# Kernel optimization log

Measured on AMD Instinct MI355X. Metric: run time of the kernel, lower is better.

Reference implementation:

```python
import jax, jax.numpy as jnp
import numpy as np

B, S, UNITS = 32, 2048, 512

def setup_inputs() -> dict:
    key = jax.random.key(0)
    ks = jax.random.split(key, 8)
    sc = 1.0 / np.sqrt(UNITS)
    return {
        "s_prev": jax.random.normal(ks[0], (B, UNITS), jnp.float32),
        "hidden_states": jax.random.normal(ks[1], (B, S, UNITS), jnp.float32),
        "W_kernel": jax.random.normal(ks[2], (UNITS, UNITS), jnp.float32) * sc,
        "W_bias": jnp.zeros((UNITS,), jnp.float32),
        "U_kernel": jax.random.normal(ks[3], (UNITS, UNITS), jnp.float32) * sc,
        "U_bias": jnp.zeros((UNITS,), jnp.float32),
        "V_kernel": jax.random.normal(ks[4], (UNITS, 1), jnp.float32) * sc,
        "V_bias": jnp.zeros((1,), jnp.float32),
    }

def reference(s_prev, hidden_states, W_kernel, W_bias, U_kernel, U_bias, V_kernel, V_bias):
    # NOTE: faithful to the source code: U is applied to s_prev, W to hidden_states,
    # and the context is computed as softmax-weights * s_prev (as written, a quirk
    # of the original module), summed over the sequence axis.
    first = s_prev @ U_kernel + U_bias                      # (B, units)
    second = hidden_states @ W_kernel + W_bias              # (B, S, units)
    score = jnp.tanh(first[:, None, :] + second) @ V_kernel + V_bias  # (B, S, 1)
    weights = jax.nn.softmax(score, axis=1)                 # (B, S, 1)
    context = jnp.sum(weights * s_prev[:, None, :], axis=1) # (B, units)
    return context, weights
```

## Files before the change

kernel.cpp:

```cpp
#include <hip/hip_runtime.h>

#define NBATCH 32
#define SEQ    2048
#define NU     512
#define ASTR   36

typedef __attribute__((ext_vector_type(8)))  short bf16x8;
typedef __attribute__((ext_vector_type(16))) float f32x16;

__device__ __forceinline__ short bf16_of(float f) {
  union { float f; unsigned u; } v; v.f = f;
  unsigned r = v.u + 0x7fffu + ((v.u >> 16) & 1u);
  return (short)(r >> 16);
}

__device__ __forceinline__ float fast_tanh(float x) {
  float ax = __builtin_fabsf(x);
  float t  = __expf(-2.0f * ax);
  float r  = (1.0f - t) / (1.0f + t);
  return x < 0.0f ? -r : r;
}

__global__ __launch_bounds__(256) void prep_w(const float* __restrict__ W,
                                              short* __restrict__ Wt) {
  int idx = blockIdx.x * 256 + threadIdx.x;
  int u = idx >> 9, k = idx & 511;
  Wt[(size_t)u * NU + k] = bf16_of(W[(size_t)k * NU + u]);
}

__global__ __launch_bounds__(256) void prep_first(const float* __restrict__ sp,
                                                  const float* __restrict__ U,
                                                  const float* __restrict__ Ub,
                                                  const float* __restrict__ Wb,
                                                  float* __restrict__ first) {
  __shared__ float srow[NU];
  int b = blockIdx.x >> 1;
  int half = blockIdx.x & 1;
  int t = threadIdx.x;
  srow[t]       = sp[b * NU + t];
  srow[t + 256] = sp[b * NU + t + 256];
  __syncthreads();
  int col = half * 256 + t;
  float acc = Ub[col] + Wb[col];
  #pragma unroll 8
  for (int k = 0; k < NU; ++k) acc += srow[k] * U[(size_t)k * NU + col];
  first[b * NU + col] = acc;
}

__global__ __launch_bounds__(256, 3) void attn_main(
    const float* __restrict__ h,
    const short* __restrict__ Wt,
    const float* __restrict__ first,
    const float* __restrict__ V,
    float* __restrict__ s0)
{
  __shared__ short Alds[2][128 * ASTR];
  __shared__ short Blds[2][128 * ASTR];
  __shared__ float scores_lds[128];

  const int tid  = threadIdx.x;
  const int lane = tid & 63;
  const int w    = tid >> 6;
  const int wr   = w >> 1, wc = w & 1;
  const int l31  = lane & 31, hi = lane >> 5;

  const int bid = blockIdx.x;
  const int lb  = (bid & 7) * 256 + (bid >> 3);
  const int panel = lb >> 2, q = lb & 3;
  const int rowbase = panel * 128;
  const int b = panel >> 4;

  const int arow  = tid >> 1;
  const int ahalf = tid & 1;
  const float* hA = h + (size_t)(rowbase + arow) * NU + ahalf * 16;
  const int awr   = arow * ASTR + ahalf * 16;
  const short* bsrc = Wt + (size_t)(q * 128 + arow) * NU + ahalf * 16;
  const int bwr   = awr;

  const int rA0 = (wr * 64 +  0 + l31) * ASTR + hi * 8;
  const int rA1 = (wr * 64 + 32 + l31) * ASTR + hi * 8;
  const int rB0 = (wc * 64 +  0 + l31) * ASTR + hi * 8;
  const int rB1 = (wc * 64 + 32 + l31) * ASTR + hi * 8;

  f32x16 acc[2][2];
  #pragma unroll
  for (int rt = 0; rt < 2; ++rt)
    #pragma unroll
    for (int ct = 0; ct < 2; ++ct)
      #pragma unroll
      for (int r = 0; r < 16; ++r) acc[rt][ct][r] = 0.f;

  float4 r0, r1, r2, r3;
  int4 q0, q1;

  r0 = *reinterpret_cast<const float4*>(hA + 0);
  r1 = *reinterpret_cast<const float4*>(hA + 4);
  r2 = *reinterpret_cast<const float4*>(hA + 8);
  r3 = *reinterpret_cast<const float4*>(hA + 12);
  q0 = *reinterpret_cast<const int4*>(bsrc + 0);
  q1 = *reinterpret_cast<const int4*>(bsrc + 8);
  {
    bf16x8 v0, v1;
    v0[0]=bf16_of(r0.x); v0[1]=bf16_of(r0.y); v0[2]=bf16_of(r0.z); v0[3]=bf16_of(r0.w);
    v0[4]=bf16_of(r1.x); v0[5]=bf16_of(r1.y); v0[6]=bf16_of(r1.z); v0[7]=bf16_of(r1.w);
    v1[0]=bf16_of(r2.x); v1[1]=bf16_of(r2.y); v1[2]=bf16_of(r2.z); v1[3]=bf16_of(r2.w);
    v1[4]=bf16_of(r3.x); v1[5]=bf16_of(r3.y); v1[6]=bf16_of(r3.z); v1[7]=bf16_of(r3.w);
    *reinterpret_cast<bf16x8*>(&Alds[0][awr])     = v0;
    *reinterpret_cast<bf16x8*>(&Alds[0][awr + 8]) = v1;
    *reinterpret_cast<int4*>(&Blds[0][bwr])       = q0;
    *reinterpret_cast<int4*>(&Blds[0][bwr + 8])   = q1;
  }
  __syncthreads();

  for (int kt = 0; kt < 16; ++kt) {
    const int cur = kt & 1;
    if (kt < 15) {
      const float* hk = hA + (kt + 1) * 32;
      r0 = *reinterpret_cast<const float4*>(hk + 0);
      r1 = *reinterpret_cast<const float4*>(hk + 4);
      r2 = *reinterpret_cast<const float4*>(hk + 8);
      r3 = *reinterpret_cast<const float4*>(hk + 12);
      const short* bk = bsrc + (kt + 1) * 32;
      q0 = *reinterpret_cast<const int4*>(bk + 0);
      q1 = *reinterpret_cast<const int4*>(bk + 8);
    }

    #pragma unroll
    for (int ks = 0; ks < 2; ++ks) {
      bf16x8 af[2], bf[2];
      af[0] = *reinterpret_cast<const bf16x8*>(&Alds[cur][rA0 + ks * 16]);
      af[1] = *reinterpret_cast<const bf16x8*>(&Alds[cur][rA1 + ks * 16]);
      bf[0] = *reinterpret_cast<const bf16x8*>(&Blds[cur][rB0 + ks * 16]);
      bf[1] = *reinterpret_cast<const bf16x8*>(&Blds[cur][rB1 + ks * 16]);
      #pragma unroll
      for (int rt = 0; rt < 2; ++rt)
        #pragma unroll
        for (int ct = 0; ct < 2; ++ct)
          acc[rt][ct] = __builtin_amdgcn_mfma_f32_32x32x16_bf16(af[rt], bf[ct], acc[rt][ct], 0, 0, 0);
    }

    if (kt < 15) {
      bf16x8 v0, v1;
      v0[0]=bf16_of(r0.x); v0[1]=bf16_of(r0.y); v0[2]=bf16_of(r0.z); v0[3]=bf16_of(r0.w);
      v0[4]=bf16_of(r1.x); v0[5]=bf16_of(r1.y); v0[6]=bf16_of(r1.z); v0[7]=bf16_of(r1.w);
      v1[0]=bf16_of(r2.x); v1[1]=bf16_of(r2.y); v1[2]=bf16_of(r2.z); v1[3]=bf16_of(r2.w);
      v1[4]=bf16_of(r3.x); v1[5]=bf16_of(r3.y); v1[6]=bf16_of(r3.z); v1[7]=bf16_of(r3.w);
      const int nxt = cur ^ 1;
      *reinterpret_cast<bf16x8*>(&Alds[nxt][awr])     = v0;
      *reinterpret_cast<bf16x8*>(&Alds[nxt][awr + 8]) = v1;
      *reinterpret_cast<int4*>(&Blds[nxt][bwr])       = q0;
      *reinterpret_cast<int4*>(&Blds[nxt][bwr + 8])   = q1;
    }
    __syncthreads();
  }

  float fv[2], vv[2];
  #pragma unroll
  for (int ct = 0; ct < 2; ++ct) {
    int col = q * 128 + wc * 64 + ct * 32 + l31;
    fv[ct] = first[b * NU + col];
    vv[ct] = V[col];
  }
  float part[2][16];
  #pragma unroll
  for (int rt = 0; rt < 2; ++rt) {
    #pragma unroll
    for (int r = 0; r < 16; ++r) {
      float p = 0.f;
      #pragma unroll
      for (int ct = 0; ct < 2; ++ct)
        p += vv[ct] * fast_tanh(fv[ct] + acc[rt][ct][r]);
      #pragma unroll
      for (int m = 1; m < 32; m <<= 1) p += __shfl_xor(p, m, 64);
      part[rt][r] = p;
    }
  }
  __syncthreads();
  if (wc == 0 && l31 == 0) {
    #pragma unroll
    for (int rt = 0; rt < 2; ++rt)
      #pragma unroll
      for (int r = 0; r < 16; ++r)
        scores_lds[wr * 64 + rt * 32 + (r & 3) + 8 * (r >> 2) + 4 * hi] = part[rt][r];
  }
  __syncthreads();
  if (wc == 1 && l31 == 0) {
    #pragma unroll
    for (int rt = 0; rt < 2; ++rt)
      #pragma unroll
      for (int r = 0; r < 16; ++r)
        scores_lds[wr * 64 + rt * 32 + (r & 3) + 8 * (r >> 2) + 4 * hi] += part[rt][r];
  }
  __syncthreads();
  if (tid < 128) atomicAdd(&s0[rowbase + tid], scores_lds[tid]);
}

__global__ __launch_bounds__(256) void softmax_ctx(const float* __restrict__ sp,
                                                   float* __restrict__ out) {
  const int b = blockIdx.x;
  const int t = threadIdx.x;
  float* wgt = out + NBATCH * NU + (size_t)b * SEQ;
  __shared__ float red[4];

  float v[8];
  float mx = -1e30f;
  #pragma unroll
  for (int i = 0; i < 8; ++i) { v[i] = wgt[t + i * 256]; mx = fmaxf(mx, v[i]); }
  #pragma unroll
  for (int m = 1; m < 64; m <<= 1) mx = fmaxf(mx, __shfl_xor(mx, m, 64));
  if ((t & 63) == 0) red[t >> 6] = mx;
  __syncthreads();
  mx = fmaxf(fmaxf(red[0], red[1]), fmaxf(red[2], red[3]));
  __syncthreads();

  float se = 0.f;
  #pragma unroll
  for (int i = 0; i < 8; ++i) { v[i] = __expf(v[i] - mx); se += v[i]; }
  #pragma unroll
  for (int m = 1; m < 64; m <<= 1) se += __shfl_xor(se, m, 64);
  if ((t & 63) == 0) red[t >> 6] = se;
  __syncthreads();
  se = red[0] + red[1] + red[2] + red[3];
  __syncthreads();

  const float inv = 1.0f / se;
  float sw = 0.f;
  #pragma unroll
  for (int i = 0; i < 8; ++i) { float wi = v[i] * inv; wgt[t + i * 256] = wi; sw += wi; }
  #pragma unroll
  for (int m = 1; m < 64; m <<= 1) sw += __shfl_xor(sw, m, 64);
  if ((t & 63) == 0) red[t >> 6] = sw;
  __syncthreads();
  sw = red[0] + red[1] + red[2] + red[3];

  out[b * NU + t]       = sp[b * NU + t] * sw;
  out[b * NU + t + 256] = sp[b * NU + t + 256] * sw;
}

extern "C" void kernel_launch(void* const* d_in, const int* in_sizes, int n_in,
                              void* d_out, int out_size, void* d_ws, size_t ws_size,
                              hipStream_t stream) {
  (void)in_sizes; (void)n_in; (void)out_size; (void)ws_size;
  const float* s_prev = (const float*)d_in[0];
  const float* h      = (const float*)d_in[1];
  const float* Wk     = (const float*)d_in[2];
  const float* Wb     = (const float*)d_in[3];
  const float* Uk     = (const float*)d_in[4];
  const float* Ub     = (const float*)d_in[5];
  const float* Vk     = (const float*)d_in[6];

  float* out   = (float*)d_out;
  float* first = (float*)d_ws;
  short* Wt    = (short*)((char*)d_ws + 65536);
  float* s0    = out + NBATCH * NU;

  hipMemsetAsync(s0, 0, (size_t)NBATCH * SEQ * sizeof(float), stream);
  prep_w     <<<1024, 256, 0, stream>>>(Wk, Wt);
  prep_first <<<  64, 256, 0, stream>>>(s_prev, Uk, Ub, Wb, first);
  attn_main  <<<2048, 256, 0, stream>>>(h, Wt, first, Vk, s0);
  softmax_ctx<<<  32, 256, 0, stream>>>(s_prev, out);
}
```

Measured before the change: 120.5 us.

## Prefetch h two tiles ahead, truncate bf16 via perm, merge prep kernels

The main GEMM loop now keeps two register sets of hidden-state data in flight, loading the tile two K-steps ahead with a manually unrolled ping-pong loop, so global-load latency is better hidden behind MFMA work. The float-to-bf16 conversion for the activations changes from round-to-nearest-even bit arithmetic to a single byte-permute truncation per pair, which cuts VALU work but lowers accuracy slightly. The two prep kernels are merged into one launch to save launch overhead. The extra prefetch registers may raise register pressure under the 3-blocks-per-CU launch bound.

```diff
diff --git a/kernel.cpp b/kernel.cpp
--- a/kernel.cpp
+++ b/kernel.cpp
@@ -8,10 +8,14 @@
 typedef __attribute__((ext_vector_type(8)))  short bf16x8;
 typedef __attribute__((ext_vector_type(16))) float f32x16;
 
-__device__ __forceinline__ short bf16_of(float f) {
+__device__ __forceinline__ short bf16_rne(float f) {
   union { float f; unsigned u; } v; v.f = f;
   unsigned r = v.u + 0x7fffu + ((v.u >> 16) & 1u);
   return (short)(r >> 16);
+}
+
+__device__ __forceinline__ unsigned pk2(float lo, float hi) {
+  return __builtin_amdgcn_perm(__float_as_uint(hi), __float_as_uint(lo), 0x07060302u);
 }
 
 __device__ __forceinline__ float fast_tanh(float x) {
@@ -21,30 +25,30 @@
   return x < 0.0f ? -r : r;
 }
 
-__global__ __launch_bounds__(256) void prep_w(const float* __restrict__ W,
-                                              short* __restrict__ Wt) {
-  int idx = blockIdx.x * 256 + threadIdx.x;
-  int u = idx >> 9, k = idx & 511;
-  Wt[(size_t)u * NU + k] = bf16_of(W[(size_t)k * NU + u]);
-}
-
-__global__ __launch_bounds__(256) void prep_first(const float* __restrict__ sp,
-                                                  const float* __restrict__ U,
-                                                  const float* __restrict__ Ub,
-                                                  const float* __restrict__ Wb,
-                                                  float* __restrict__ first) {
+__global__ __launch_bounds__(256) void prep_all(const float* __restrict__ W,
+                                                const float* __restrict__ sp,
+                                                const float* __restrict__ U,
+                                                const float* __restrict__ Ub,
+                                                const float* __restrict__ Wb,
+                                                short* __restrict__ Wt,
+                                                float* __restrict__ first) {
   __shared__ float srow[NU];
-  int b = blockIdx.x >> 1;
-  int half = blockIdx.x & 1;
-  int t = threadIdx.x;
-  srow[t]       = sp[b * NU + t];
-  srow[t + 256] = sp[b * NU + t + 256];
-  __syncthreads();
-  int col = half * 256 + t;
-  float acc = Ub[col] + Wb[col];
-  #pragma unroll 8
-  for (int k = 0; k < NU; ++k) acc += srow[k] * U[(size_t)k * NU + col];
-  first[b * NU + col] = acc;
+  if (blockIdx.x < 1024) {
+    int idx = blockIdx.x * 256 + threadIdx.x;
+    int u = idx >> 9, k = idx & 511;
+    Wt[(size_t)u * NU + k] = bf16_rne(W[(size_t)k * NU + u]);
+  } else {
+    int blk = blockIdx.x - 1024;
+    int b = blk >> 1, half = blk & 1, t = threadIdx.x;
+    srow[t]       = sp[b * NU + t];
+    srow[t + 256] = sp[b * NU + t + 256];
+    __syncthreads();
+    int col = half * 256 + t;
+    float acc = Ub[col] + Wb[col];
+    #pragma unroll 8
+    for (int k = 0; k < NU; ++k) acc += srow[k] * U[(size_t)k * NU + col];
+    first[b * NU + col] = acc;
+  }
 }
 
 __global__ __launch_bounds__(256, 3) void attn_main(
@@ -75,7 +79,6 @@
   const float* hA = h + (size_t)(rowbase + arow) * NU + ahalf * 16;
   const int awr   = arow * ASTR + ahalf * 16;
   const short* bsrc = Wt + (size_t)(q * 128 + arow) * NU + ahalf * 16;
-  const int bwr   = awr;
 
   const int rA0 = (wr * 64 +  0 + l31) * ASTR + hi * 8;
   const int rA1 = (wr * 64 + 32 + l31) * ASTR + hi * 8;
@@ -90,69 +93,89 @@
       #pragma unroll
       for (int r = 0; r < 16; ++r) acc[rt][ct][r] = 0.f;
 
-  float4 r0, r1, r2, r3;
-  int4 q0, q1;
-
-  r0 = *reinterpret_cast<const float4*>(hA + 0);
-  r1 = *reinterpret_cast<const float4*>(hA + 4);
-  r2 = *reinterpret_cast<const float4*>(hA + 8);
-  r3 = *reinterpret_cast<const float4*>(hA + 12);
-  q0 = *reinterpret_cast<const int4*>(bsrc + 0);
-  q1 = *reinterpret_cast<const int4*>(bsrc + 8);
-  {
-    bf16x8 v0, v1;
-    v0[0]=bf16_of(r0.x); v0[1]=bf16_of(r0.y); v0[2]=bf16_of(r0.z); v0[3]=bf16_of(r0.w);
-    v0[4]=bf16_of(r1.x); v0[5]=bf16_of(r1.y); v0[6]=bf16_of(r1.z); v0[7]=bf16_of(r1.w);
-    v1[0]=bf16_of(r2.x); v1[1]=bf16_of(r2.y); v1[2]=bf16_of(r2.z); v1[3]=bf16_of(r2.w);
-    v1[4]=bf16_of(r3.x); v1[5]=bf16_of(r3.y); v1[6]=bf16_of(r3.z); v1[7]=bf16_of(r3.w);
-    *reinterpret_cast<bf16x8*>(&Alds[0][awr])     = v0;
-    *reinterpret_cast<bf16x8*>(&Alds[0][awr + 8]) = v1;
-    *reinterpret_cast<int4*>(&Blds[0][bwr])       = q0;
-    *reinterpret_cast<int4*>(&Blds[0][bwr + 8])   = q1;
-  }
-  __syncthreads();
-
-  for (int kt = 0; kt < 16; ++kt) {
-    const int cur = kt & 1;
-    if (kt < 15) {
-      const float* hk = hA + (kt + 1) * 32;
-      r0 = *reinterpret_cast<const float4*>(hk + 0);
-      r1 = *reinterpret_cast<const float4*>(hk + 4);
-      r2 = *reinterpret_cast<const float4*>(hk + 8);
-      r3 = *reinterpret_cast<const float4*>(hk + 12);
-      const short* bk = bsrc + (kt + 1) * 32;
-      q0 = *reinterpret_cast<const int4*>(bk + 0);
-      q1 = *reinterpret_cast<const int4*>(bk + 8);
-    }
-
-    #pragma unroll
-    for (int ks = 0; ks < 2; ++ks) {
-      bf16x8 af[2], bf[2];
-      af[0] = *reinterpret_cast<const bf16x8*>(&Alds[cur][rA0 + ks * 16]);
-      af[1] = *reinterpret_cast<const bf16x8*>(&Alds[cur][rA1 + ks * 16]);
-      bf[0] = *reinterpret_cast<const bf16x8*>(&Blds[cur][rB0 + ks * 16]);
-      bf[1] = *reinterpret_cast<const bf16x8*>(&Blds[cur][rB1 + ks * 16]);
-      #pragma unroll
-      for (int rt = 0; rt < 2; ++rt)
-        #pragma unroll
-        for (int ct = 0; ct < 2; ++ct)
-          acc[rt][ct] = __builtin_amdgcn_mfma_f32_32x32x16_bf16(af[rt], bf[ct], acc[rt][ct], 0, 0, 0);
-    }
-
-    if (kt < 15) {
-      bf16x8 v0, v1;
-      v0[0]=bf16_of(r0.x); v0[1]=bf16_of(r0.y); v0[2]=bf16_of(r0.z); v0[3]=bf16_of(r0.w);
-      v0[4]=bf16_of(r1.x); v0[5]=bf16_of(r1.y); v0[6]=bf16_of(r1.z); v0[7]=bf16_of(r1.w);
-      v1[0]=bf16_of(r2.x); v1[1]=bf16_of(r2.y); v1[2]=bf16_of(r2.z); v1[3]=bf16_of(r2.w);
-      v1[4]=bf16_of(r3.x); v1[5]=bf16_of(r3.y); v1[6]=bf16_of(r3.z); v1[7]=bf16_of(r3.w);
-      const int nxt = cur ^ 1;
-      *reinterpret_cast<bf16x8*>(&Alds[nxt][awr])     = v0;
-      *reinterpret_cast<bf16x8*>(&Alds[nxt][awr + 8]) = v1;
-      *reinterpret_cast<int4*>(&Blds[nxt][bwr])       = q0;
-      *reinterpret_cast<int4*>(&Blds[nxt][bwr + 8])   = q1;
-    }
+  float4 ha0, ha1, ha2, ha3;
+  float4 hb0, hb1, hb2, hb3;
+  int4   bq0, bq1;
+
+  #define CVT_WRITE(dst, H0, H1, H2, H3)                                   \
+    {                                                                      \
+      uint4 u0, u1;                                                        \
+      u0.x = pk2(H0.x, H0.y); u0.y = pk2(H0.z, H0.w);                      \
+      u0.z = pk2(H1.x, H1.y); u0.w = pk2(H1.z, H1.w);                      \
+      u1.x = pk2(H2.x, H2.y); u1.y = pk2(H2.z, H2.w);                      \
+      u1.z = pk2(H3.x, H3.y); u1.w = pk2(H3.z, H3.w);                      \
+      *reinterpret_cast<uint4*>(&Alds[dst][awr])     = u0;                 \
+      *reinterpret_cast<uint4*>(&Alds[dst][awr + 8]) = u1;                 \
+      *reinterpret_cast<int4*>(&Blds[dst][awr])      = bq0;                \
+      *reinterpret_cast<int4*>(&Blds[dst][awr + 8])  = bq1;                \
+    }
+
+  #define COMPUTE(cur)                                                     \
+    _Pragma("unroll")                                                      \
+    for (int ks = 0; ks < 2; ++ks) {                                       \
+      bf16x8 af0, af1, bf0, bf1;                                           \
+      af0 = *reinterpret_cast<const bf16x8*>(&Alds[cur][rA0 + ks * 16]);   \
+      af1 = *reinterpret_cast<const bf16x8*>(&Alds[cur][rA1 + ks * 16]);   \
+      bf0 = *reinterpret_cast<const bf16x8*>(&Blds[cur][rB0 + ks * 16]);   \
+      bf1 = *reinterpret_cast<const bf16x8*>(&Blds[cur][rB1 + ks * 16]);   \
+      acc[0][0] = __builtin_amdgcn_mfma_f32_32x32x16_bf16(af0, bf0, acc[0][0], 0, 0, 0); \
+      acc[0][1] = __builtin_amdgcn_mfma_f32_32x32x16_bf16(af0, bf1, acc[0][1], 0, 0, 0); \
+      acc[1][0] = __builtin_amdgcn_mfma_f32_32x32x16_bf16(af1, bf0, acc[1][0], 0, 0, 0); \
+      acc[1][1] = __builtin_amdgcn_mfma_f32_32x32x16_bf16(af1, bf1, acc[1][1], 0, 0, 0); \
+    }
+
+  bq0 = *reinterpret_cast<const int4*>(bsrc);
+  bq1 = *reinterpret_cast<const int4*>(bsrc + 8);
+  ha0 = *reinterpret_cast<const float4*>(hA + 0);
+  ha1 = *reinterpret_cast<const float4*>(hA + 4);
+  ha2 = *reinterpret_cast<const float4*>(hA + 8);
+  ha3 = *reinterpret_cast<const float4*>(hA + 12);
+  CVT_WRITE(0, ha0, ha1, ha2, ha3);
+  hb0 = *reinterpret_cast<const float4*>(hA + 32);
+  hb1 = *reinterpret_cast<const float4*>(hA + 36);
+  hb2 = *reinterpret_cast<const float4*>(hA + 40);
+  hb3 = *reinterpret_cast<const float4*>(hA + 44);
+  __syncthreads();
+
+  for (int kt2 = 0; kt2 < 7; ++kt2) {
+    const int kt = kt2 * 2;
+    bq0 = *reinterpret_cast<const int4*>(bsrc + (kt + 1) * 32);
+    bq1 = *reinterpret_cast<const int4*>(bsrc + (kt + 1) * 32 + 8);
+    {
+      const float* p = hA + (kt + 2) * 32;
+      ha0 = *reinterpret_cast<const float4*>(p + 0);
+      ha1 = *reinterpret_cast<const float4*>(p + 4);
+      ha2 = *reinterpret_cast<const float4*>(p + 8);
+      ha3 = *reinterpret_cast<const float4*>(p + 12);
+    }
+    COMPUTE(0);
+    CVT_WRITE(1, hb0, hb1, hb2, hb3);
     __syncthreads();
-  }
+
+    bq0 = *reinterpret_cast<const int4*>(bsrc + (kt + 2) * 32);
+    bq1 = *reinterpret_cast<const int4*>(bsrc + (kt + 2) * 32 + 8);
+    {
+      const float* p = hA + (kt + 3) * 32;
+      hb0 = *reinterpret_cast<const float4*>(p + 0);
+      hb1 = *reinterpret_cast<const float4*>(p + 4);
+      hb2 = *reinterpret_cast<const float4*>(p + 8);
+      hb3 = *reinterpret_cast<const float4*>(p + 12);
+    }
+    COMPUTE(1);
+    CVT_WRITE(0, ha0, ha1, ha2, ha3);
+    __syncthreads();
+  }
+
+  bq0 = *reinterpret_cast<const int4*>(bsrc + 15 * 32);
+  bq1 = *reinterpret_cast<const int4*>(bsrc + 15 * 32 + 8);
+  COMPUTE(0);
+  CVT_WRITE(1, hb0, hb1, hb2, hb3);
+  __syncthreads();
+
+  COMPUTE(1);
+
+  #undef CVT_WRITE
+  #undef COMPUTE
 
   float fv[2], vv[2];
   #pragma unroll
@@ -255,8 +278,7 @@
   float* s0    = out + NBATCH * NU;
 
   hipMemsetAsync(s0, 0, (size_t)NBATCH * SEQ * sizeof(float), stream);
-  prep_w     <<<1024, 256, 0, stream>>>(Wk, Wt);
-  prep_first <<<  64, 256, 0, stream>>>(s_prev, Uk, Ub, Wb, first);
+  prep_all   <<<1088, 256, 0, stream>>>(Wk, s_prev, Uk, Ub, Wb, Wt, first);
   attn_main  <<<2048, 256, 0, stream>>>(h, Wt, first, Vk, s0);
   softmax_ctx<<<  32, 256, 0, stream>>>(s_prev, out);
 }
```

Measured after the change: 113.5 us. -5.8%, faster.
